# Performance work log

Hardware: AMD Instinct MI355X
Metric: run time of the kernel (lower is better)

Reference implementation:

```python
import jax, jax.numpy as jnp
import numpy as np


def _dot_prod_attention(h, enc):
    # h: (B,T,H), enc: (B,S,H) used as both keys and values
    att = jnp.einsum('bth,bsh->bts', h, enc)      # (B,T,S)
    att = jax.nn.softmax(att, axis=-1)
    ctx = jnp.einsum('bts,bsh->bth', att, enc)    # (B,T,H)
    return ctx, att


def setup_inputs() -> dict:
    key = jax.random.key(0)
    ks = jax.random.split(key, 7)
    B, T, S, St, H = 8, 1024, 1024, 512, 1024
    scale = 1.0 / np.sqrt(H)
    return {
        'output': jax.random.normal(ks[0], (B, T, H), dtype=jnp.float32),
        'sent': jax.random.normal(ks[1], (B, S, H), dtype=jnp.float32),
        'template': jax.random.normal(ks[2], (B, St, H), dtype=jnp.float32),
        'W_gate': jax.random.normal(ks[3], (H, 3 * H), dtype=jnp.float32) * scale,
        'W_sent': jax.random.normal(ks[4], (H, H), dtype=jnp.float32) * scale,
        'W_template': jax.random.normal(ks[5], (H, H), dtype=jnp.float32) * scale,
        'W_output': jax.random.normal(ks[6], (H, H), dtype=jnp.float32) * scale,
    }


def reference(output, sent, template, W_gate, W_sent, W_template, W_output):
    sent_ctx, sent_weight = _dot_prod_attention(output, sent)
    template_ctx, template_weight = _dot_prod_attention(output, template)

    cat = jnp.concatenate([sent_ctx, template_ctx, output], axis=-1)  # (B,T,3H)
    gate = jax.nn.sigmoid(jnp.einsum('btk,hk->bth', cat, W_gate))     # (B,T,H)

    fusion = ((1.0 - gate) * jnp.einsum('bth,kh->btk', sent_ctx, W_sent)
              + gate * jnp.einsum('bth,kh->btk', template_ctx, W_template)
              + jnp.einsum('bth,kh->btk', output, W_output))
    fusion = jnp.tanh(fusion)
    return fusion, sent_weight, template_weight
```

## Files before the change

### kernel.cpp

```cpp
#include <hip/hip_runtime.h>
#include <stdint.h>

typedef unsigned short u16;
typedef float f32x4 __attribute__((ext_vector_type(4)));
typedef int   i32x4 __attribute__((ext_vector_type(4)));

__device__ __forceinline__ u16 f2h(float f) {
  _Float16 h = (_Float16)f;
  u16 u; __builtin_memcpy(&u, &h, 2); return u;
}
__device__ __forceinline__ float h2f(u16 u) {
  _Float16 h; __builtin_memcpy(&h, &u, 2); return (float)h;
}

__device__ __forceinline__ void mfma_f16(f32x4& c, i32x4 a, i32x4 b) {
  asm("v_mfma_f32_16x16x32_f16 %0, %1, %2, %0" : "+v"(c) : "v"(a), "v"(b));
}

__device__ __forceinline__ void g2l16(const u16* g, u16* l) {
  __builtin_amdgcn_global_load_lds((const __attribute__((address_space(1))) void*)g,
                                   (__attribute__((address_space(3))) void*)l,
                                   16, 0, 0);
}

__device__ __forceinline__ void xcd_swz(int& bx, int& by, int& bz) {
  const int gx = gridDim.x, gy = gridDim.y;
  const int n = gx * gy * gridDim.z;
  const int lin = blockIdx.x + gx * (blockIdx.y + gy * blockIdx.z);
  const int q = n >> 3;
  const int s = (lin & 7) * q + (lin >> 3);
  bx = s % gx;
  const int t = s / gx;
  by = t % gy;
  bz = t / gy;
}

struct alignas(8) US4 { u16 a, b, c, d; };

__global__ void k_conv_hilo(const float* __restrict__ src, u16* __restrict__ hi,
                            u16* __restrict__ lo, int n4) {
  int i = blockIdx.x * blockDim.x + threadIdx.x;
  int stride = gridDim.x * blockDim.x;
  for (; i < n4; i += stride) {
    float4 v = reinterpret_cast<const float4*>(src)[i];
    US4 h, l;
    h.a = f2h(v.x); l.a = f2h(v.x - h2f(h.a));
    h.b = f2h(v.y); l.b = f2h(v.y - h2f(h.b));
    h.c = f2h(v.z); l.c = f2h(v.z - h2f(h.c));
    h.d = f2h(v.w); l.d = f2h(v.w - h2f(h.d));
    reinterpret_cast<US4*>(hi)[i] = h;
    reinterpret_cast<US4*>(lo)[i] = l;
  }
}

__global__ void k_conv_w(const float* __restrict__ s_wg, const float* __restrict__ s_ws,
                         const float* __restrict__ s_wt, const float* __restrict__ s_wo,
                         u16* __restrict__ d_wg, u16* __restrict__ d_ws,
                         u16* __restrict__ d_wt, u16* __restrict__ d_wo) {
  constexpr int N1 = 786432;
  constexpr int N2 = 262144;
  constexpr int total = N1 + 3 * N2;
  int i = blockIdx.x * blockDim.x + threadIdx.x;
  int stride = gridDim.x * blockDim.x;
  for (; i < total; i += stride) {
    const float* s; u16* d; int j;
    if (i < N1)                { s = s_wg; d = d_wg; j = i; }
    else if (i < N1 + N2)      { s = s_ws; d = d_ws; j = i - N1; }
    else if (i < N1 + 2 * N2)  { s = s_wt; d = d_wt; j = i - N1 - N2; }
    else                       { s = s_wo; d = d_wo; j = i - N1 - 2 * N2; }
    float4 v = reinterpret_cast<const float4*>(s)[j];
    US4 h; h.a = f2h(v.x); h.b = f2h(v.y); h.c = f2h(v.z); h.d = f2h(v.w);
    reinterpret_cast<US4*>(d)[j] = h;
  }
}

__global__ __launch_bounds__(256)
void k_conv_T(const float* __restrict__ src, u16* __restrict__ dh, u16* __restrict__ dl,
              u16* __restrict__ dt, int R, int C) {
  __shared__ u16 t[32][33];
  const int b = blockIdx.z;
  const float* s = src + (size_t)b * R * C;
  u16* dhb = dh + (size_t)b * R * C;
  u16* dlb = dl + (size_t)b * R * C;
  u16* dtb = dt + (size_t)b * R * C;
  const int c0 = blockIdx.x * 32, r0 = blockIdx.y * 32;
  const int tx = threadIdx.x, ty = threadIdx.y;
#pragma unroll
  for (int j = ty; j < 32; j += 8) {
    const size_t idx = (size_t)(r0 + j) * C + (c0 + tx);
    float x = s[idx];
    u16 h = f2h(x);
    dhb[idx] = h;
    dlb[idx] = f2h(x - h2f(h));
    t[j][tx] = h;
  }
  __syncthreads();
#pragma unroll
  for (int j = ty; j < 32; j += 8)
    dtb[(size_t)(c0 + j) * R + (r0 + tx)] = t[tx][j];
}

template<int L>
__global__ __launch_bounds__(256)
void k_softmax(float* __restrict__ io, u16* __restrict__ pb) {
  const int lane = threadIdx.x & 63;
  const size_t r = (size_t)blockIdx.x * 4 + (threadIdx.x >> 6);
  float* row = io + r * L;
  u16* prow = pb + r * L;
  constexpr int NV = L / 64;
  float v[NV];
  float mx = -3.4e38f;
#pragma unroll
  for (int j = 0; j < NV; ++j) { v[j] = row[lane + j * 64]; mx = fmaxf(mx, v[j]); }
#pragma unroll
  for (int s = 32; s; s >>= 1) mx = fmaxf(mx, __shfl_xor(mx, s));
  float sum = 0.f;
#pragma unroll
  for (int j = 0; j < NV; ++j) { v[j] = __expf(v[j] - mx); sum += v[j]; }
#pragma unroll
  for (int s = 32; s; s >>= 1) sum += __shfl_xor(sum, s);
  const float inv = 1.f / sum;
#pragma unroll
  for (int j = 0; j < NV; ++j) {
    float pv = v[j] * inv;
    row[lane + j * 64] = pv;
    prow[lane + j * 64] = f2h(pv);
  }
}

constexpr int BM = 128, BN = 128, BK = 32;

struct TC { int wv, sr, sc, wm, wn, fr, kq; };

__device__ __forceinline__ TC make_tc(int tid) {
  TC t;
  const int lane = tid & 63;
  t.wv = tid >> 6;
  t.sr = lane >> 2;
  t.sc = (lane & 3) * 8;
  t.wm = t.wv >> 1;
  t.wn = t.wv & 1;
  t.fr = lane & 15;
  t.kq = (lane >> 4) * 8;
  return t;
}

template<int SPLIT>
__device__ __forceinline__ void gemm_pass(
    f32x4 (&acc)[16],
    const u16* __restrict__ A, const u16* __restrict__ Al, int lda,
    const u16* __restrict__ B, const u16* __restrict__ Bl, int ldb,
    int K, u16* sA, u16* sAl, u16* sB, u16* sBl, const TC& t)
{
  const int nt = K / BK;
  auto stage = [&](int c, int k0) {
    u16* dA = sA + c * (BM * BK);
    u16* dB = sB + c * (BN * BK);
    const u16* ar = A + (size_t)t.sr * lda + k0 + t.sc;
    const u16* br = B + (size_t)t.sr * ldb + k0 + t.sc;
    g2l16(ar + (size_t)(t.wv * 16) * lda, dA + (t.wv * 16) * BK);
    g2l16(ar + (size_t)((t.wv + 4) * 16) * lda, dA + ((t.wv + 4) * 16) * BK);
    g2l16(br + (size_t)(t.wv * 16) * ldb, dB + (t.wv * 16) * BK);
    g2l16(br + (size_t)((t.wv + 4) * 16) * ldb, dB + ((t.wv + 4) * 16) * BK);
    if constexpr (SPLIT) {
      u16* dAl = sAl + c * (BM * BK);
      u16* dBl = sBl + c * (BN * BK);
      const u16* alr = Al + (size_t)t.sr * lda + k0 + t.sc;
      const u16* blr = Bl + (size_t)t.sr * ldb + k0 + t.sc;
      g2l16(alr + (size_t)(t.wv * 16) * lda, dAl + (t.wv * 16) * BK);
      g2l16(alr + (size_t)((t.wv + 4) * 16) * lda, dAl + ((t.wv + 4) * 16) * BK);
      g2l16(blr + (size_t)(t.wv * 16) * ldb, dBl + (t.wv * 16) * BK);
      g2l16(blr + (size_t)((t.wv + 4) * 16) * ldb, dBl + ((t.wv + 4) * 16) * BK);
    }
  };

  stage(0, 0);
  __syncthreads();
  int c = 0;
  for (int it = 0; it < nt; ++it) {
    if (it + 1 < nt) stage(c ^ 1, (it + 1) * BK);
    const u16* bA = sA + c * (BM * BK);
    const u16* bB = sB + c * (BN * BK);
    i32x4 ah[4], bh[4];
#pragma unroll
    for (int i = 0; i < 4; ++i) {
      ah[i] = *reinterpret_cast<const i32x4*>(&bA[(t.wm * 64 + i * 16 + t.fr) * BK + t.kq]);
      bh[i] = *reinterpret_cast<const i32x4*>(&bB[(t.wn * 64 + i * 16 + t.fr) * BK + t.kq]);
    }
    if constexpr (SPLIT) {
      const u16* bAl = sAl + c * (BM * BK);
      const u16* bBl = sBl + c * (BN * BK);
      i32x4 al[4], bl[4];
#pragma unroll
      for (int i = 0; i < 4; ++i) {
        al[i] = *reinterpret_cast<const i32x4*>(&bAl[(t.wm * 64 + i * 16 + t.fr) * BK + t.kq]);
        bl[i] = *reinterpret_cast<const i32x4*>(&bBl[(t.wn * 64 + i * 16 + t.fr) * BK + t.kq]);
      }
#pragma unroll
      for (int i = 0; i < 4; ++i)
#pragma unroll
        for (int j = 0; j < 4; ++j) {
          mfma_f16(acc[i * 4 + j], ah[i], bh[j]);
          mfma_f16(acc[i * 4 + j], al[i], bh[j]);
          mfma_f16(acc[i * 4 + j], ah[i], bl[j]);
        }
    } else {
#pragma unroll
      for (int i = 0; i < 4; ++i)
#pragma unroll
        for (int j = 0; j < 4; ++j)
          mfma_f16(acc[i * 4 + j], ah[i], bh[j]);
    }
    __syncthreads();
    c ^= 1;
  }
}

template<int SPLIT, int EPI>
__global__ __launch_bounds__(256, 2)
void k_gemm_nt(const u16* __restrict__ A0, const u16* __restrict__ A1, const u16* __restrict__ A2,
               const u16* __restrict__ Alo,
               const u16* __restrict__ Bm, const u16* __restrict__ Blo,
               int lda, int ldb, long long strA, long long strB,
               float* __restrict__ Cf, u16* __restrict__ Cb, int ldc, long long strC,
               int segK, int nseg)
{
  __shared__ __align__(16) u16 sA[2 * BM * BK];
  __shared__ __align__(16) u16 sB[2 * BN * BK];
  __shared__ __align__(16) u16 sAl[SPLIT ? 2 * BM * BK : 8];
  __shared__ __align__(16) u16 sBl[SPLIT ? 2 * BN * BK : 8];

  int bx, by, bz;
  xcd_swz(bx, by, bz);
  const TC t = make_tc(threadIdx.x);

  const size_t aoff = (size_t)((long long)bz * strA) + (size_t)by * BM * lda;
  const size_t boff = (size_t)((long long)bz * strB) + (size_t)bx * BN * ldb;

  f32x4 acc[16];
#pragma unroll
  for (int i = 0; i < 16; ++i) acc[i] = f32x4{0.f, 0.f, 0.f, 0.f};

  const u16* As[3] = {A0, A1, A2};
  for (int s = 0; s < nseg; ++s) {
    gemm_pass<SPLIT>(acc, As[s] + aoff, SPLIT ? Alo + aoff : nullptr, lda,
                     Bm + boff + (size_t)s * segK, SPLIT ? Blo + boff : nullptr, ldb,
                     segK, sA, sAl, sB, sBl, t);
  }

  const size_t cbse = (size_t)((long long)bz * strC);
  const int row0 = by * BM + t.wm * 64;
  const int col0 = bx * BN + t.wn * 64;
  const int fq = ((threadIdx.x & 63) >> 4) * 4;
#pragma unroll
  for (int i = 0; i < 4; ++i) {
#pragma unroll
    for (int j = 0; j < 4; ++j) {
      f32x4 v = acc[i * 4 + j];
      const int c = col0 + j * 16 + t.fr;
#pragma unroll
      for (int q = 0; q < 4; ++q) {
        const int r = row0 + i * 16 + fq + q;
        const size_t idx = cbse + (size_t)r * ldc + c;
        if constexpr (EPI == 0) {
          Cf[idx] = v[q];
        } else if constexpr (EPI == 2) {
          Cb[idx] = f2h(v[q]);
        } else {
          Cb[idx] = f2h(1.f / (1.f + __expf(-v[q])));
        }
      }
    }
  }
}

__global__ __launch_bounds__(256, 2)
void k_fusion(const u16* __restrict__ ctx_s, const u16* __restrict__ ctx_t,
              const u16* __restrict__ outh,
              const u16* __restrict__ Ws, const u16* __restrict__ Wt,
              const u16* __restrict__ Wo,
              const u16* __restrict__ g16, float* __restrict__ fus)
{
  constexpr int H = 1024;
  __shared__ __align__(16) u16 sA[2 * BM * BK];
  __shared__ __align__(16) u16 sB[2 * BN * BK];

  int bx, by, bz;
  xcd_swz(bx, by, bz);
  const TC t = make_tc(threadIdx.x);

  const size_t aoff = (size_t)by * BM * H;
  const size_t boff = (size_t)bx * BN * H;

  const int row0 = by * BM + t.wm * 64;
  const int col0 = bx * BN + t.wn * 64;
  const int fq = ((threadIdx.x & 63) >> 4) * 4;

  f32x4 acc[16];
#pragma unroll
  for (int i = 0; i < 16; ++i) acc[i] = f32x4{0.f, 0.f, 0.f, 0.f};

  gemm_pass<0>(acc, ctx_s + aoff, nullptr, H, Ws + boff, nullptr, H, H,
               sA, nullptr, sB, nullptr, t);
  f32x4 S[16];
#pragma unroll
  for (int i = 0; i < 16; ++i) { S[i] = acc[i]; acc[i] = f32x4{0.f, 0.f, 0.f, 0.f}; }

  gemm_pass<0>(acc, ctx_t + aoff, nullptr, H, Wt + boff, nullptr, H, H,
               sA, nullptr, sB, nullptr, t);
#pragma unroll
  for (int i = 0; i < 4; ++i) {
#pragma unroll
    for (int j = 0; j < 4; ++j) {
      const int c = col0 + j * 16 + t.fr;
#pragma unroll
      for (int q = 0; q < 4; ++q) {
        const int r = row0 + i * 16 + fq + q;
        const float gv = h2f(g16[(size_t)r * H + c]);
        const float sv = S[i * 4 + j][q];
        S[i * 4 + j][q] = sv + gv * (acc[i * 4 + j][q] - sv);
      }
    }
  }
#pragma unroll
  for (int i = 0; i < 16; ++i) acc[i] = f32x4{0.f, 0.f, 0.f, 0.f};

  gemm_pass<0>(acc, outh + aoff, nullptr, H, Wo + boff, nullptr, H, H,
               sA, nullptr, sB, nullptr, t);
#pragma unroll
  for (int i = 0; i < 4; ++i) {
#pragma unroll
    for (int j = 0; j < 4; ++j) {
      const int c = col0 + j * 16 + t.fr;
#pragma unroll
      for (int q = 0; q < 4; ++q) {
        const int r = row0 + i * 16 + fq + q;
        float x = S[i * 4 + j][q] + acc[i * 4 + j][q];
        float ax = fabsf(x);
        float e = __expf(-2.f * ax);
        float th = (1.f - e) / (1.f + e);
        fus[(size_t)r * H + c] = copysignf(th, x);
      }
    }
  }
}

extern "C" void kernel_launch(void* const* d_in, const int* in_sizes, int n_in,
                              void* d_out, int out_size, void* d_ws, size_t ws_size,
                              hipStream_t stream) {
  (void)in_sizes; (void)n_in; (void)out_size; (void)ws_size;
  constexpr int B = 8, T = 1024, S = 1024, St = 512, H = 1024;
  constexpr long long BTH = (long long)B * T * H;
  constexpr long long BSH = (long long)B * S * H;
  constexpr long long BStH = (long long)B * St * H;
  constexpr long long BTS = (long long)B * T * S;
  constexpr long long BTSt = (long long)B * T * St;
  constexpr long long TH = (long long)T * H;

  const float* in_out  = (const float*)d_in[0];
  const float* in_sent = (const float*)d_in[1];
  const float* in_tmpl = (const float*)d_in[2];
  const float* in_Wg   = (const float*)d_in[3];
  const float* in_Ws   = (const float*)d_in[4];
  const float* in_Wt   = (const float*)d_in[5];
  const float* in_Wo   = (const float*)d_in[6];

  float* fus = (float*)d_out;
  float* sw  = fus + BTH;
  float* tw  = sw + BTS;

  char* p = (char*)d_ws;
  auto take = [&](long long bytes) { char* q = p; p += bytes; return q; };
  u16* out_h   = (u16*)take(BTH * 2);
  u16* out_lo  = (u16*)take(BTH * 2);
  u16* sent_h  = (u16*)take(BSH * 2);
  u16* sent_lo = (u16*)take(BSH * 2);
  u16* tmpl_h  = (u16*)take(BStH * 2);
  u16* tmpl_lo = (u16*)take(BStH * 2);
  u16* sentT   = (u16*)take(BSH * 2);
  u16* tmplT   = (u16*)take(BStH * 2);
  u16* Wg_h    = (u16*)take((long long)3 * H * H * 2);
  u16* Ws_h    = (u16*)take((long long)H * H * 2);
  u16* Wt_h    = (u16*)take((long long)H * H * 2);
  u16* Wo_h    = (u16*)take((long long)H * H * 2);
  u16* Ps      = (u16*)take(BTS * 2);
  u16* Pt      = (u16*)take(BTSt * 2);
  u16* g16     = (u16*)take(BTH * 2);

  u16* ctx_s = sent_h;
  u16* ctx_t = sent_lo;

  dim3 thr(256);

  k_conv_hilo<<<2048, 256, 0, stream>>>(in_out, out_h, out_lo, (int)(BTH / 4));
  k_conv_w<<<1024, 256, 0, stream>>>(in_Wg, in_Ws, in_Wt, in_Wo, Wg_h, Ws_h, Wt_h, Wo_h);
  k_conv_T<<<dim3(H / 32, S / 32, B), dim3(32, 8), 0, stream>>>(in_sent, sent_h, sent_lo, sentT, S, H);
  k_conv_T<<<dim3(H / 32, St / 32, B), dim3(32, 8), 0, stream>>>(in_tmpl, tmpl_h, tmpl_lo, tmplT, St, H);

  k_gemm_nt<1, 0><<<dim3(S / BN, T / BM, B), thr, 0, stream>>>(
      out_h, nullptr, nullptr, out_lo, sent_h, sent_lo, H, H, TH, (long long)S * H,
      sw, nullptr, S, (long long)T * S, H, 1);
  k_gemm_nt<1, 0><<<dim3(St / BN, T / BM, B), thr, 0, stream>>>(
      out_h, nullptr, nullptr, out_lo, tmpl_h, tmpl_lo, H, H, TH, (long long)St * H,
      tw, nullptr, St, (long long)T * St, H, 1);

  k_softmax<1024><<<(B * T) / 4, 256, 0, stream>>>(sw, Ps);
  k_softmax<512><<<(B * T) / 4, 256, 0, stream>>>(tw, Pt);

  k_gemm_nt<0, 2><<<dim3(H / BN, T / BM, B), thr, 0, stream>>>(
      Ps, nullptr, nullptr, nullptr, sentT, nullptr, S, S, (long long)T * S, (long long)H * S,
      nullptr, ctx_s, H, TH, S, 1);
  k_gemm_nt<0, 2><<<dim3(H / BN, T / BM, B), thr, 0, stream>>>(
      Pt, nullptr, nullptr, nullptr, tmplT, nullptr, St, St, (long long)T * St, (long long)H * St,
      nullptr, ctx_t, H, TH, St, 1);

  k_gemm_nt<0, 6><<<dim3(H / BN, (B * T) / BM, 1), thr, 0, stream>>>(
      ctx_s, ctx_t, out_h, nullptr, Wg_h, nullptr, H, 3 * H, 0LL, 0LL,
      nullptr, g16, H, 0LL, H, 3);

  k_fusion<<<dim3(H / BN, (B * T) / BM, 1), thr, 0, stream>>>(
      ctx_s, ctx_t, out_h, Ws_h, Wt_h, Wo_h, g16, fus);
}
```

Measured before the change: 407.8 us.

## Fuse gate GEMM into fusion kernel, use BK=64 passes and column-major XCD swizzle

The gate GEMM (sigmoid of cat·Wg) moves into the fusion kernel. Its sigmoid result is kept in registers as fp16, so the g16 intermediate is no longer written to and re-read from global memory and one kernel launch goes away. The non-split GEMMs (PV and fusion) now stage 64-wide K tiles, which halves the number of barriers per K. The fusion grid uses a column-grouped XCD swizzle so that blocks on the same XCD share weight tiles. MFMA calls now use the compiler builtin instead of inline asm, which lets the compiler schedule them, but the doubled LDS per block and the extra live gate registers may reduce occupancy.

```diff
diff --git a/kernel.cpp b/kernel.cpp
--- a/kernel.cpp
+++ b/kernel.cpp
@@ -2,8 +2,9 @@
 #include <stdint.h>
 
 typedef unsigned short u16;
-typedef float f32x4 __attribute__((ext_vector_type(4)));
-typedef int   i32x4 __attribute__((ext_vector_type(4)));
+typedef float    f32x4 __attribute__((ext_vector_type(4)));
+typedef _Float16 f16x8 __attribute__((ext_vector_type(8)));
+typedef _Float16 f16x4 __attribute__((ext_vector_type(4)));
 
 __device__ __forceinline__ u16 f2h(float f) {
   _Float16 h = (_Float16)f;
@@ -13,8 +14,8 @@
   _Float16 h; __builtin_memcpy(&h, &u, 2); return (float)h;
 }
 
-__device__ __forceinline__ void mfma_f16(f32x4& c, i32x4 a, i32x4 b) {
-  asm("v_mfma_f32_16x16x32_f16 %0, %1, %2, %0" : "+v"(c) : "v"(a), "v"(b));
+__device__ __forceinline__ void mfma_f16(f32x4& c, f16x8 a, f16x8 b) {
+  c = __builtin_amdgcn_mfma_f32_16x16x32_f16(a, b, c, 0, 0, 0);
 }
 
 __device__ __forceinline__ void g2l16(const u16* g, u16* l) {
@@ -23,16 +24,26 @@
                                    16, 0, 0);
 }
 
-__device__ __forceinline__ void xcd_swz(int& bx, int& by, int& bz) {
+__device__ __forceinline__ void xcd_batch(int& bx, int& by, int& bz) {
   const int gx = gridDim.x, gy = gridDim.y;
   const int n = gx * gy * gridDim.z;
   const int lin = blockIdx.x + gx * (blockIdx.y + gy * blockIdx.z);
   const int q = n >> 3;
   const int s = (lin & 7) * q + (lin >> 3);
   bx = s % gx;
-  const int t = s / gx;
-  by = t % gy;
-  bz = t / gy;
+  const int t2 = s / gx;
+  by = t2 % gy;
+  bz = t2 / gy;
+}
+
+__device__ __forceinline__ void xcd_col(int& bx, int& by) {
+  const int gx = gridDim.x, gy = gridDim.y;
+  const int n = gx * gy;
+  const int cpx = n >> 3;
+  const int lin = blockIdx.x + gx * blockIdx.y;
+  const int s = (lin & 7) * cpx + (lin >> 3);
+  bx = s / gy;
+  by = s % gy;
 }
 
 struct alignas(8) US4 { u16 a, b, c, d; };
@@ -128,8 +139,6 @@
   }
 }
 
-constexpr int BM = 128, BN = 128, BK = 32;
-
 struct TC { int wv, sr, sc, wm, wn, fr, kq; };
 
 __device__ __forceinline__ TC make_tc(int tid) {
@@ -145,190 +154,229 @@
   return t;
 }
 
-template<int SPLIT>
-__device__ __forceinline__ void gemm_pass(
+constexpr int SUB = 128 * 32;
+
+__device__ __forceinline__ void pass64(
+    f32x4 (&acc)[16],
+    const u16* __restrict__ A, int lda,
+    const u16* __restrict__ B, int ldb,
+    int K, u16* sA, u16* sB, const TC& t)
+{
+  const int nt = K / 64;
+  auto stage = [&](int c, int k0) {
+#pragma unroll
+    for (int sub = 0; sub < 2; ++sub) {
+      u16* dA = sA + c * (2 * SUB) + sub * SUB;
+      u16* dB = sB + c * (2 * SUB) + sub * SUB;
+      const u16* ar = A + (size_t)t.sr * lda + k0 + sub * 32 + t.sc;
+      const u16* br = B + (size_t)t.sr * ldb + k0 + sub * 32 + t.sc;
+      g2l16(ar + (size_t)(t.wv * 16) * lda, dA + (t.wv * 16) * 32);
+      g2l16(ar + (size_t)((t.wv + 4) * 16) * lda, dA + ((t.wv + 4) * 16) * 32);
+      g2l16(br + (size_t)(t.wv * 16) * ldb, dB + (t.wv * 16) * 32);
+      g2l16(br + (size_t)((t.wv + 4) * 16) * ldb, dB + ((t.wv + 4) * 16) * 32);
+    }
+  };
+
+  stage(0, 0);
+  __syncthreads();
+  int c = 0;
+  for (int it = 0; it < nt; ++it) {
+    if (it + 1 < nt) stage(c ^ 1, (it + 1) * 64);
+#pragma unroll
+    for (int sub = 0; sub < 2; ++sub) {
+      const u16* bA = sA + c * (2 * SUB) + sub * SUB;
+      const u16* bB = sB + c * (2 * SUB) + sub * SUB;
+      f16x8 ah[4], bh[4];
+#pragma unroll
+      for (int i = 0; i < 4; ++i) {
+        ah[i] = *reinterpret_cast<const f16x8*>(&bA[(t.wm * 64 + i * 16 + t.fr) * 32 + t.kq]);
+        bh[i] = *reinterpret_cast<const f16x8*>(&bB[(t.wn * 64 + i * 16 + t.fr) * 32 + t.kq]);
+      }
+#pragma unroll
+      for (int i = 0; i < 4; ++i)
+#pragma unroll
+        for (int j = 0; j < 4; ++j)
+          mfma_f16(acc[i * 4 + j], ah[i], bh[j]);
+    }
+    __syncthreads();
+    c ^= 1;
+  }
+}
+
+__device__ __forceinline__ void pass32s(
     f32x4 (&acc)[16],
     const u16* __restrict__ A, const u16* __restrict__ Al, int lda,
     const u16* __restrict__ B, const u16* __restrict__ Bl, int ldb,
     int K, u16* sA, u16* sAl, u16* sB, u16* sBl, const TC& t)
 {
-  const int nt = K / BK;
+  const int nt = K / 32;
   auto stage = [&](int c, int k0) {
-    u16* dA = sA + c * (BM * BK);
-    u16* dB = sB + c * (BN * BK);
+    u16* dA = sA + c * SUB;  u16* dB = sB + c * SUB;
+    u16* dAl = sAl + c * SUB; u16* dBl = sBl + c * SUB;
     const u16* ar = A + (size_t)t.sr * lda + k0 + t.sc;
     const u16* br = B + (size_t)t.sr * ldb + k0 + t.sc;
-    g2l16(ar + (size_t)(t.wv * 16) * lda, dA + (t.wv * 16) * BK);
-    g2l16(ar + (size_t)((t.wv + 4) * 16) * lda, dA + ((t.wv + 4) * 16) * BK);
-    g2l16(br + (size_t)(t.wv * 16) * ldb, dB + (t.wv * 16) * BK);
-    g2l16(br + (size_t)((t.wv + 4) * 16) * ldb, dB + ((t.wv + 4) * 16) * BK);
-    if constexpr (SPLIT) {
-      u16* dAl = sAl + c * (BM * BK);
-      u16* dBl = sBl + c * (BN * BK);
-      const u16* alr = Al + (size_t)t.sr * lda + k0 + t.sc;
-      const u16* blr = Bl + (size_t)t.sr * ldb + k0 + t.sc;
-      g2l16(alr + (size_t)(t.wv * 16) * lda, dAl + (t.wv * 16) * BK);
-      g2l16(alr + (size_t)((t.wv + 4) * 16) * lda, dAl + ((t.wv + 4) * 16) * BK);
-      g2l16(blr + (size_t)(t.wv * 16) * ldb, dBl + (t.wv * 16) * BK);
-      g2l16(blr + (size_t)((t.wv + 4) * 16) * ldb, dBl + ((t.wv + 4) * 16) * BK);
-    }
+    const u16* alr = Al + (size_t)t.sr * lda + k0 + t.sc;
+    const u16* blr = Bl + (size_t)t.sr * ldb + k0 + t.sc;
+    g2l16(ar + (size_t)(t.wv * 16) * lda, dA + (t.wv * 16) * 32);
+    g2l16(ar + (size_t)((t.wv + 4) * 16) * lda, dA + ((t.wv + 4) * 16) * 32);
+    g2l16(br + (size_t)(t.wv * 16) * ldb, dB + (t.wv * 16) * 32);
+    g2l16(br + (size_t)((t.wv + 4) * 16) * ldb, dB + ((t.wv + 4) * 16) * 32);
+    g2l16(alr + (size_t)(t.wv * 16) * lda, dAl + (t.wv * 16) * 32);
+    g2l16(alr + (size_t)((t.wv + 4) * 16) * lda, dAl + ((t.wv + 4) * 16) * 32);
+    g2l16(blr + (size_t)(t.wv * 16) * ldb, dBl + (t.wv * 16) * 32);
+    g2l16(blr + (size_t)((t.wv + 4) * 16) * ldb, dBl + ((t.wv + 4) * 16) * 32);
   };
 
   stage(0, 0);
   __syncthreads();
   int c = 0;
   for (int it = 0; it < nt; ++it) {
-    if (it + 1 < nt) stage(c ^ 1, (it + 1) * BK);
-    const u16* bA = sA + c * (BM * BK);
-    const u16* bB = sB + c * (BN * BK);
-    i32x4 ah[4], bh[4];
+    if (it + 1 < nt) stage(c ^ 1, (it + 1) * 32);
+    const u16* bA = sA + c * SUB;  const u16* bB = sB + c * SUB;
+    const u16* bAl = sAl + c * SUB; const u16* bBl = sBl + c * SUB;
+    f16x8 ah[4], bh[4], al[4], bl[4];
 #pragma unroll
     for (int i = 0; i < 4; ++i) {
-      ah[i] = *reinterpret_cast<const i32x4*>(&bA[(t.wm * 64 + i * 16 + t.fr) * BK + t.kq]);
-      bh[i] = *reinterpret_cast<const i32x4*>(&bB[(t.wn * 64 + i * 16 + t.fr) * BK + t.kq]);
-    }
-    if constexpr (SPLIT) {
-      const u16* bAl = sAl + c * (BM * BK);
-      const u16* bBl = sBl + c * (BN * BK);
-      i32x4 al[4], bl[4];
-#pragma unroll
-      for (int i = 0; i < 4; ++i) {
-        al[i] = *reinterpret_cast<const i32x4*>(&bAl[(t.wm * 64 + i * 16 + t.fr) * BK + t.kq]);
-        bl[i] = *reinterpret_cast<const i32x4*>(&bBl[(t.wn * 64 + i * 16 + t.fr) * BK + t.kq]);
+      ah[i] = *reinterpret_cast<const f16x8*>(&bA[(t.wm * 64 + i * 16 + t.fr) * 32 + t.kq]);
+      bh[i] = *reinterpret_cast<const f16x8*>(&bB[(t.wn * 64 + i * 16 + t.fr) * 32 + t.kq]);
+      al[i] = *reinterpret_cast<const f16x8*>(&bAl[(t.wm * 64 + i * 16 + t.fr) * 32 + t.kq]);
+      bl[i] = *reinterpret_cast<const f16x8*>(&bBl[(t.wn * 64 + i * 16 + t.fr) * 32 + t.kq]);
+    }
+#pragma unroll
+    for (int i = 0; i < 4; ++i)
+#pragma unroll
+      for (int j = 0; j < 4; ++j) {
+        mfma_f16(acc[i * 4 + j], ah[i], bh[j]);
+        mfma_f16(acc[i * 4 + j], al[i], bh[j]);
+        mfma_f16(acc[i * 4 + j], ah[i], bl[j]);
       }
-#pragma unroll
-      for (int i = 0; i < 4; ++i)
-#pragma unroll
-        for (int j = 0; j < 4; ++j) {
-          mfma_f16(acc[i * 4 + j], ah[i], bh[j]);
-          mfma_f16(acc[i * 4 + j], al[i], bh[j]);
-          mfma_f16(acc[i * 4 + j], ah[i], bl[j]);
-        }
-    } else {
-#pragma unroll
-      for (int i = 0; i < 4; ++i)
-#pragma unroll
-        for (int j = 0; j < 4; ++j)
-          mfma_f16(acc[i * 4 + j], ah[i], bh[j]);
-    }
     __syncthreads();
     c ^= 1;
   }
 }
 
-template<int SPLIT, int EPI>
 __global__ __launch_bounds__(256, 2)
-void k_gemm_nt(const u16* __restrict__ A0, const u16* __restrict__ A1, const u16* __restrict__ A2,
-               const u16* __restrict__ Alo,
-               const u16* __restrict__ Bm, const u16* __restrict__ Blo,
-               int lda, int ldb, long long strA, long long strB,
-               float* __restrict__ Cf, u16* __restrict__ Cb, int ldc, long long strC,
-               int segK, int nseg)
+void k_logits(const u16* __restrict__ Ah, const u16* __restrict__ Al,
+              const u16* __restrict__ Bh, const u16* __restrict__ Bl,
+              long long strB, float* __restrict__ Cf, int ldc, long long strC)
 {
-  __shared__ __align__(16) u16 sA[2 * BM * BK];
-  __shared__ __align__(16) u16 sB[2 * BN * BK];
-  __shared__ __align__(16) u16 sAl[SPLIT ? 2 * BM * BK : 8];
-  __shared__ __align__(16) u16 sBl[SPLIT ? 2 * BN * BK : 8];
-
+  __shared__ __align__(16) u16 sA[2 * SUB], sB[2 * SUB], sAl[2 * SUB], sBl[2 * SUB];
   int bx, by, bz;
-  xcd_swz(bx, by, bz);
+  xcd_batch(bx, by, bz);
   const TC t = make_tc(threadIdx.x);
 
-  const size_t aoff = (size_t)((long long)bz * strA) + (size_t)by * BM * lda;
-  const size_t boff = (size_t)((long long)bz * strB) + (size_t)bx * BN * ldb;
+  const size_t aoff = (size_t)bz * (1024 * 1024) + (size_t)by * 128 * 1024;
+  const size_t boff = (size_t)bz * strB + (size_t)bx * 128 * 1024;
 
   f32x4 acc[16];
 #pragma unroll
   for (int i = 0; i < 16; ++i) acc[i] = f32x4{0.f, 0.f, 0.f, 0.f};
 
-  const u16* As[3] = {A0, A1, A2};
-  for (int s = 0; s < nseg; ++s) {
-    gemm_pass<SPLIT>(acc, As[s] + aoff, SPLIT ? Alo + aoff : nullptr, lda,
-                     Bm + boff + (size_t)s * segK, SPLIT ? Blo + boff : nullptr, ldb,
-                     segK, sA, sAl, sB, sBl, t);
-  }
-
-  const size_t cbse = (size_t)((long long)bz * strC);
-  const int row0 = by * BM + t.wm * 64;
-  const int col0 = bx * BN + t.wn * 64;
+  pass32s(acc, Ah + aoff, Al + aoff, 1024, Bh + boff, Bl + boff, 1024, 1024,
+          sA, sAl, sB, sBl, t);
+
+  const size_t cbse = (size_t)bz * strC;
+  const int row0 = by * 128 + t.wm * 64;
+  const int col0 = bx * 128 + t.wn * 64;
   const int fq = ((threadIdx.x & 63) >> 4) * 4;
 #pragma unroll
-  for (int i = 0; i < 4; ++i) {
+  for (int i = 0; i < 4; ++i)
 #pragma unroll
     for (int j = 0; j < 4; ++j) {
-      f32x4 v = acc[i * 4 + j];
       const int c = col0 + j * 16 + t.fr;
 #pragma unroll
-      for (int q = 0; q < 4; ++q) {
-        const int r = row0 + i * 16 + fq + q;
-        const size_t idx = cbse + (size_t)r * ldc + c;
-        if constexpr (EPI == 0) {
-          Cf[idx] = v[q];
-        } else if constexpr (EPI == 2) {
-          Cb[idx] = f2h(v[q]);
-        } else {
-          Cb[idx] = f2h(1.f / (1.f + __expf(-v[q])));
-        }
-      }
-    }
-  }
+      for (int q = 0; q < 4; ++q)
+        Cf[cbse + (size_t)(row0 + i * 16 + fq + q) * ldc + c] = acc[i * 4 + j][q];
+    }
 }
 
 __global__ __launch_bounds__(256, 2)
-void k_fusion(const u16* __restrict__ ctx_s, const u16* __restrict__ ctx_t,
-              const u16* __restrict__ outh,
-              const u16* __restrict__ Ws, const u16* __restrict__ Wt,
-              const u16* __restrict__ Wo,
-              const u16* __restrict__ g16, float* __restrict__ fus)
+void k_pv(const u16* __restrict__ A, const u16* __restrict__ Bt, int ld,
+          long long strA, long long strB, u16* __restrict__ Cb, long long strC)
+{
+  __shared__ __align__(16) u16 sA[2 * 2 * SUB], sB[2 * 2 * SUB];
+  int bx, by, bz;
+  xcd_batch(bx, by, bz);
+  const TC t = make_tc(threadIdx.x);
+
+  f32x4 acc[16];
+#pragma unroll
+  for (int i = 0; i < 16; ++i) acc[i] = f32x4{0.f, 0.f, 0.f, 0.f};
+
+  pass64(acc, A + (size_t)bz * strA + (size_t)by * 128 * ld, ld,
+         Bt + (size_t)bz * strB + (size_t)bx * 128 * ld, ld, ld, sA, sB, t);
+
+  const size_t cbse = (size_t)bz * strC;
+  const int row0 = by * 128 + t.wm * 64;
+  const int col0 = bx * 128 + t.wn * 64;
+  const int fq = ((threadIdx.x & 63) >> 4) * 4;
+#pragma unroll
+  for (int i = 0; i < 4; ++i)
+#pragma unroll
+    for (int j = 0; j < 4; ++j) {
+      const int c = col0 + j * 16 + t.fr;
+#pragma unroll
+      for (int q = 0; q < 4; ++q)
+        Cb[cbse + (size_t)(row0 + i * 16 + fq + q) * 1024 + c] = f2h(acc[i * 4 + j][q]);
+    }
+}
+
+__global__ __launch_bounds__(256, 2)
+void k_fusion4(const u16* __restrict__ ctx_s, const u16* __restrict__ ctx_t,
+               const u16* __restrict__ outh,
+               const u16* __restrict__ Wg, const u16* __restrict__ Ws,
+               const u16* __restrict__ Wt, const u16* __restrict__ Wo,
+               float* __restrict__ fus)
 {
   constexpr int H = 1024;
-  __shared__ __align__(16) u16 sA[2 * BM * BK];
-  __shared__ __align__(16) u16 sB[2 * BN * BK];
-
-  int bx, by, bz;
-  xcd_swz(bx, by, bz);
+  __shared__ __align__(16) u16 sA[2 * 2 * SUB], sB[2 * 2 * SUB];
+
+  int bx, by;
+  xcd_col(bx, by);
   const TC t = make_tc(threadIdx.x);
 
-  const size_t aoff = (size_t)by * BM * H;
-  const size_t boff = (size_t)bx * BN * H;
-
-  const int row0 = by * BM + t.wm * 64;
-  const int col0 = bx * BN + t.wn * 64;
+  const size_t aoff = (size_t)by * 128 * H;
+  const int row0 = by * 128 + t.wm * 64;
+  const int col0 = bx * 128 + t.wn * 64;
   const int fq = ((threadIdx.x & 63) >> 4) * 4;
 
   f32x4 acc[16];
 #pragma unroll
   for (int i = 0; i < 16; ++i) acc[i] = f32x4{0.f, 0.f, 0.f, 0.f};
 
-  gemm_pass<0>(acc, ctx_s + aoff, nullptr, H, Ws + boff, nullptr, H, H,
-               sA, nullptr, sB, nullptr, t);
+  const u16* As[3] = {ctx_s, ctx_t, outh};
+  for (int s = 0; s < 3; ++s)
+    pass64(acc, As[s] + aoff, H, Wg + (size_t)bx * 128 * (3 * H) + s * H, 3 * H, H,
+           sA, sB, t);
+  f16x4 gh[16];
+#pragma unroll
+  for (int f = 0; f < 16; ++f)
+#pragma unroll
+    for (int q = 0; q < 4; ++q)
+      gh[f][q] = (_Float16)(1.f / (1.f + __expf(-acc[f][q])));
+
+#pragma unroll
+  for (int i = 0; i < 16; ++i) acc[i] = f32x4{0.f, 0.f, 0.f, 0.f};
+  pass64(acc, ctx_s + aoff, H, Ws + (size_t)bx * 128 * H, H, H, sA, sB, t);
   f32x4 S[16];
 #pragma unroll
   for (int i = 0; i < 16; ++i) { S[i] = acc[i]; acc[i] = f32x4{0.f, 0.f, 0.f, 0.f}; }
 
-  gemm_pass<0>(acc, ctx_t + aoff, nullptr, H, Wt + boff, nullptr, H, H,
-               sA, nullptr, sB, nullptr, t);
-#pragma unroll
-  for (int i = 0; i < 4; ++i) {
-#pragma unroll
-    for (int j = 0; j < 4; ++j) {
-      const int c = col0 + j * 16 + t.fr;
-#pragma unroll
-      for (int q = 0; q < 4; ++q) {
-        const int r = row0 + i * 16 + fq + q;
-        const float gv = h2f(g16[(size_t)r * H + c]);
-        const float sv = S[i * 4 + j][q];
-        S[i * 4 + j][q] = sv + gv * (acc[i * 4 + j][q] - sv);
-      }
-    }
-  }
+  pass64(acc, ctx_t + aoff, H, Wt + (size_t)bx * 128 * H, H, H, sA, sB, t);
+#pragma unroll
+  for (int f = 0; f < 16; ++f)
+#pragma unroll
+    for (int q = 0; q < 4; ++q) {
+      const float gv = (float)gh[f][q];
+      const float sv = S[f][q];
+      S[f][q] = sv + gv * (acc[f][q] - sv);
+    }
 #pragma unroll
   for (int i = 0; i < 16; ++i) acc[i] = f32x4{0.f, 0.f, 0.f, 0.f};
 
-  gemm_pass<0>(acc, outh + aoff, nullptr, H, Wo + boff, nullptr, H, H,
-               sA, nullptr, sB, nullptr, t);
-#pragma unroll
-  for (int i = 0; i < 4; ++i) {
+  pass64(acc, outh + aoff, H, Wo + (size_t)bx * 128 * H, H, H, sA, sB, t);
+#pragma unroll
+  for (int i = 0; i < 4; ++i)
 #pragma unroll
     for (int j = 0; j < 4; ++j) {
       const int c = col0 + j * 16 + t.fr;
@@ -342,7 +390,6 @@
         fus[(size_t)r * H + c] = copysignf(th, x);
       }
     }
-  }
 }
 
 extern "C" void kernel_launch(void* const* d_in, const int* in_sizes, int n_in,
@@ -385,7 +432,6 @@
   u16* Wo_h    = (u16*)take((long long)H * H * 2);
   u16* Ps      = (u16*)take(BTS * 2);
   u16* Pt      = (u16*)take(BTSt * 2);
-  u16* g16     = (u16*)take(BTH * 2);
 
   u16* ctx_s = sent_h;
   u16* ctx_t = sent_lo;
@@ -397,27 +443,19 @@
   k_conv_T<<<dim3(H / 32, S / 32, B), dim3(32, 8), 0, stream>>>(in_sent, sent_h, sent_lo, sentT, S, H);
   k_conv_T<<<dim3(H / 32, St / 32, B), dim3(32, 8), 0, stream>>>(in_tmpl, tmpl_h, tmpl_lo, tmplT, St, H);
 
-  k_gemm_nt<1, 0><<<dim3(S / BN, T / BM, B), thr, 0, stream>>>(
-      out_h, nullptr, nullptr, out_lo, sent_h, sent_lo, H, H, TH, (long long)S * H,
-      sw, nullptr, S, (long long)T * S, H, 1);
-  k_gemm_nt<1, 0><<<dim3(St / BN, T / BM, B), thr, 0, stream>>>(
-      out_h, nullptr, nullptr, out_lo, tmpl_h, tmpl_lo, H, H, TH, (long long)St * H,
-      tw, nullptr, St, (long long)T * St, H, 1);
+  k_logits<<<dim3(S / 128, T / 128, B), thr, 0, stream>>>(
+      out_h, out_lo, sent_h, sent_lo, (long long)S * H, sw, S, (long long)T * S);
+  k_logits<<<dim3(St / 128, T / 128, B), thr, 0, stream>>>(
+      out_h, out_lo, tmpl_h, tmpl_lo, (long long)St * H, tw, St, (long long)T * St);
 
   k_softmax<1024><<<(B * T) / 4, 256, 0, stream>>>(sw, Ps);
   k_softmax<512><<<(B * T) / 4, 256, 0, stream>>>(tw, Pt);
 
-  k_gemm_nt<0, 2><<<dim3(H / BN, T / BM, B), thr, 0, stream>>>(
-      Ps, nullptr, nullptr, nullptr, sentT, nullptr, S, S, (long long)T * S, (long long)H * S,
-      nullptr, ctx_s, H, TH, S, 1);
-  k_gemm_nt<0, 2><<<dim3(H / BN, T / BM, B), thr, 0, stream>>>(
-      Pt, nullptr, nullptr, nullptr, tmplT, nullptr, St, St, (long long)T * St, (long long)H * St,
-      nullptr, ctx_t, H, TH, St, 1);
-
-  k_gemm_nt<0, 6><<<dim3(H / BN, (B * T) / BM, 1), thr, 0, stream>>>(
-      ctx_s, ctx_t, out_h, nullptr, Wg_h, nullptr, H, 3 * H, 0LL, 0LL,
-      nullptr, g16, H, 0LL, H, 3);
-
-  k_fusion<<<dim3(H / BN, (B * T) / BM, 1), thr, 0, stream>>>(
-      ctx_s, ctx_t, out_h, Ws_h, Wt_h, Wo_h, g16, fus);
-}
+  k_pv<<<dim3(H / 128, T / 128, B), thr, 0, stream>>>(
+      Ps, sentT, S, (long long)T * S, (long long)H * S, ctx_s, TH);
+  k_pv<<<dim3(H / 128, T / 128, B), thr, 0, stream>>>(
+      Pt, tmplT, St, (long long)T * St, (long long)H * St, ctx_t, TH);
+
+  k_fusion4<<<dim3(H / 128, (B * T) / 128), thr, 0, stream>>>(
+      ctx_s, ctx_t, out_h, Wg_h, Ws_h, Wt_h, Wo_h, fus);
+}
```

After: 401.2 us. About the same (-1.6%).
